# Performance work log

Hardware: AMD Instinct MI355X
Metric: run time of the kernel (lower is better)

## Reference

```python
import jax, jax.numpy as jnp
import numpy as np

jax.config.update("jax_enable_x64", True)  # loss accumulates int64 squared index diffs (~1e14)

PATCH, STRIDE = 7, 1


def extract_patches(img, p, s):
    # img: [b, c, h, w] -> patches [b, N, c*p*p], N = oh*ow (normalize_patch='none')
    pat = jax.lax.conv_general_dilated_patches(img, (p, p), (s, s), 'VALID')  # [b, c*p*p, oh, ow]
    b, d = pat.shape[0], pat.shape[1]
    return pat.reshape(b, d, -1).transpose(0, 2, 1)


def bisect_left(a, v):
    # Exact replica of np.searchsorted(a, v, side='left') binary search,
    # applied (as in the original code) to an UNSORTED int array `a`.
    # a: [N] int, v: [M] int -> [M] insertion indices in [0, N].
    N = a.shape[0]
    lo = jnp.zeros(v.shape, jnp.int64)
    hi = jnp.full(v.shape, N, jnp.int64)
    n_iter = int(np.ceil(np.log2(N))) + 1
    for _ in range(n_iter):
        mid = (lo + hi) // 2
        am = a[jnp.clip(mid, 0, N - 1)]
        go = lo < hi
        pred = am < v
        lo = jnp.where(go & pred, mid + 1, lo)
        hi = jnp.where(go & (~pred), mid, hi)
    return lo


def nearest_vals(a, v):
    # Vectorized find_nearest(a, v_i) for all v_i. a: [N], v: [M].
    N = a.shape[0]
    idx = bisect_left(a, v)
    a_prev = a[jnp.clip(idx - 1, 0, N - 1)]
    a_at = a[jnp.clip(idx, 0, N - 1)]
    take_prev = (idx > 0) & ((idx == N) | (jnp.abs(v - a_prev) < jnp.abs(v - a_at)))
    return jnp.where(take_prev, a_prev, a_at)


def reference(x, y, rand):
    # rand: [b, d, num_proj]; per-batch projection matrix, normalized by unbiased column std
    rand = rand / jnp.std(rand, axis=1, keepdims=True, ddof=1)
    xp = extract_patches(x, PATCH, STRIDE)  # [b, N, d]
    yp = extract_patches(y, PATCH, STRIDE)  # [b, N, d]
    proj_x = jnp.einsum('bnd,bdp->bnp', xp, rand)
    proj_y = jnp.einsum('bnd,bdp->bnp', yp, rand)
    # Original overwrites projections with argsort indices; only j=0 is used
    # because of the early return inside the projection loop.
    ai = jnp.argsort(proj_x[:, :, 0], axis=1).astype(jnp.int64)  # [b, N]
    at = jnp.argsort(proj_y[:, :, 0], axis=1).astype(jnp.int64)  # [b, N]
    nearest = jax.vmap(nearest_vals)(at, ai)  # [b, N]
    N = ai.shape[1]
    per_image = jnp.sum((ai - nearest) ** 2, axis=1) / N  # int sum -> float
    return jnp.mean(per_image)  # batch_reduction='mean'


def setup_inputs() -> dict:
    key = jax.random.key(0)
    k1, k2, k3 = jax.random.split(key, 3)
    b, c, h, w = 4, 3, 256, 256
    d = c * PATCH * PATCH  # 147
    x = jax.random.normal(k1, (b, c, h, w), dtype=jnp.float32)
    y = jax.random.normal(k2, (b, c, h, w), dtype=jnp.float32)
    rand = jax.random.normal(k3, (b, d, 1), dtype=jnp.float32)
    return {"x": x, "y": y, "rand": rand}
```

## Files before the change

kernel.cpp:

```cpp
#include <hip/hip_runtime.h>
#include <stdint.h>

#define OH 250
#define OW 250
#define NPTS (OH*OW)
#define NSEG 4
#define D 147
#define CH 3
#define IMH 256
#define IMW 256
#define NITER 17
#define NBUCK 4096
#define CAP 256
#define SIG0 12.124355652982141

typedef unsigned long long u64;
typedef unsigned int u32;

#define OFF_SREC  0UL
#define OFF_A     33554432UL
#define OFF_CTRL  34554432UL
#define OFF_CURS  34554432UL
#define OFF_SUMS  34619968UL
#define OFF_OFLOW 34620000UL
#define CTRL_LEN  65572UL
#define OFF_BASES 34620008UL
#define WS_NEED   34685560UL

__device__ __forceinline__ u64 packd(double f) {
  u64 u = (u64)__double_as_longlong(f);
  return (u & 0x8000000000000000ULL) ? ~u : (u | 0x8000000000000000ULL);
}

__device__ __forceinline__ int bucket_of(u64 rec) {
  u64 t = rec & ~0x1FFFFULL;
  u64 bits = (t & 0x8000000000000000ULL) ? (t & 0x7FFFFFFFFFFFFFFFULL) : ~t;
  double v = __longlong_as_double((long long)bits);
  double z = (v + 4.0 * SIG0) * ((double)NBUCK / (8.0 * SIG0));
  int b = (z <= 0.0) ? 0 : (int)z;
  if (b > NBUCK - 1) b = NBUCK - 1;
  return b;
}

__global__ __launch_bounds__(256) void conv_kern(const float* __restrict__ y,
                                                 const float* __restrict__ rnd,
                                                 u64* __restrict__ srec,
                                                 u32* __restrict__ curs,
                                                 u32* __restrict__ oflow) {
  __shared__ float tile[CH][22][22];
  __shared__ double w[D];
  int b = blockIdx.z;
  const float* in = y + (size_t)b * CH * IMH * IMW;
  int bi = blockIdx.y * 16, bj = blockIdx.x * 16;
  int tid = threadIdx.y * 16 + threadIdx.x;
  int lane = tid & 63;

  {
    double v0 = (double)rnd[b * D + lane];
    double v1 = (double)rnd[b * D + lane + 64];
    double v2 = (lane + 128 < D) ? (double)rnd[b * D + lane + 128] : 0.0;
    double sm = v0 + v1 + v2;
    #pragma unroll
    for (int o = 32; o > 0; o >>= 1) sm += __shfl_xor(sm, o, 64);
    double mean = sm / (double)D;
    double d0 = v0 - mean, d1 = v1 - mean;
    double d2 = (lane + 128 < D) ? (v2 - mean) : 0.0;
    double ss = d0 * d0 + d1 * d1 + d2 * d2;
    #pragma unroll
    for (int o = 32; o > 0; o >>= 1) ss += __shfl_xor(ss, o, 64);
    double stdv = sqrt(ss / (double)(D - 1));
    w[lane] = v0 / stdv;
    w[lane + 64] = v1 / stdv;
    if (lane + 128 < D) w[lane + 128] = v2 / stdv;
  }
  for (int c = 0; c < CH; ++c)
    for (int t = tid; t < 22 * 22; t += 256) {
      int rr = t / 22, cc = t - rr * 22;
      int r = bi + rr, col = bj + cc;
      float v = 0.f;
      if (r < IMH && col < IMW) v = in[((size_t)c * IMH + r) * IMW + col];
      tile[c][rr][cc] = v;
    }
  __syncthreads();
  int i = bi + threadIdx.y, j = bj + threadIdx.x;
  if (i < OH && j < OW) {
    double acc = 0.0;
    #pragma unroll
    for (int c = 0; c < CH; ++c)
      #pragma unroll
      for (int ph = 0; ph < 7; ++ph)
        #pragma unroll
        for (int pw = 0; pw < 7; ++pw)
          acc = fma((double)tile[c][threadIdx.y + ph][threadIdx.x + pw],
                    w[c * 49 + ph * 7 + pw], acc);
    int n = i * OW + j;
    u64 rec = (packd(acc) & ~0x1FFFFULL) | (u64)(u32)n;
    int bk = b * NBUCK + bucket_of(rec);
    u32 pos = atomicAdd(&curs[bk], 1u);
    if (pos < CAP) srec[(size_t)bk * CAP + pos] = rec;
    else atomicOr(oflow, 1u);
  }
}

__global__ __launch_bounds__(1024) void scan_kern(const u32* __restrict__ curs,
                                                  u32* __restrict__ bases) {
  __shared__ u32 part[1024];
  int seg = blockIdx.x, t = threadIdx.x;
  u32 c[4];
  #pragma unroll
  for (int m = 0; m < 4; ++m) {
    u32 v = curs[seg * NBUCK + 4 * t + m];
    c[m] = v > CAP ? CAP : v;
  }
  u32 s = c[0] + c[1] + c[2] + c[3];
  part[t] = s;
  __syncthreads();
  for (int off = 1; off < 1024; off <<= 1) {
    u32 v = (t >= off) ? part[t - off] : 0u;
    __syncthreads();
    part[t] += v;
    __syncthreads();
  }
  u32 ex = part[t] - s;
  #pragma unroll
  for (int m = 0; m < 4; ++m) {
    bases[seg * (NBUCK + 1) + 4 * t + m] = ex;
    ex += c[m];
  }
  if (t == 1023) bases[seg * (NBUCK + 1) + NBUCK] = ex;
}

__global__ __launch_bounds__(512) void bsort_kern(const u64* __restrict__ srec,
                                                  const u32* __restrict__ bases,
                                                  u32* __restrict__ a) {
  __shared__ u64 buf[8][CAP];
  int wid = threadIdx.x >> 6, lane = threadIdx.x & 63;
  int B = blockIdx.x * 8 + wid;
  int seg = B >> 12, bk = B & (NBUCK - 1);
  u32 b0 = bases[seg * (NBUCK + 1) + bk];
  u32 b1 = bases[seg * (NBUCK + 1) + bk + 1];
  int n = (int)(b1 - b0);
  const u64* src = srec + (size_t)B * CAP;
  u32* dst = a + (size_t)seg * NPTS + b0;
  for (int i = lane; i < n; i += 64) buf[wid][i] = src[i];
  __syncthreads();
  for (int i = lane; i < n; i += 64) {
    u64 x = buf[wid][i];
    int r = 0;
    for (int j = 0; j < n; ++j) r += (buf[wid][j] < x);
    dst[r] = (u32)(x & 0x1FFFFULL);
  }
}

#define HALF (NSEG * NPTS / 2)
__global__ __launch_bounds__(256) void loss_kern(const u32* __restrict__ a_all,
                                                 u64* __restrict__ sums) {
  __shared__ u64 lsums[NSEG];
  int tid = threadIdx.x;
  if (tid < NSEG) lsums[tid] = 0ULL;
  __syncthreads();
  int g = blockIdx.x * 256 + tid;
  if (g < HALF) {
    int g1 = g + HALF;
    int s0 = g / NPTS, s1 = g1 / NPTS;
    int vv0 = g - s0 * NPTS, vv1 = g1 - s1 * NPTS;
    const u32* A0 = a_all + (size_t)s0 * NPTS;
    const u32* A1 = a_all + (size_t)s1 * NPTS;
    int lo0 = 0, hi0 = NPTS, lo1 = 0, hi1 = NPTS;
    #pragma unroll
    for (int it = 0; it < NITER; ++it) {
      int mid0 = (lo0 + hi0) >> 1, mid1 = (lo1 + hi1) >> 1;
      int cm0 = mid0 > NPTS - 1 ? NPTS - 1 : mid0;
      int cm1 = mid1 > NPTS - 1 ? NPTS - 1 : mid1;
      int am0 = (int)A0[cm0];
      int am1 = (int)A1[cm1];
      if (lo0 < hi0) { if (am0 < vv0) lo0 = mid0 + 1; else hi0 = mid0; }
      if (lo1 < hi1) { if (am1 < vv1) lo1 = mid1 + 1; else hi1 = mid1; }
    }
    {
      int pi = lo0 - 1; if (pi < 0) pi = 0; if (pi > NPTS - 1) pi = NPTS - 1;
      int ci = lo0;     if (ci > NPTS - 1) ci = NPTS - 1;
      int ap = (int)A0[pi], aa = (int)A0[ci];
      int d1 = vv0 - ap; if (d1 < 0) d1 = -d1;
      int d2 = vv0 - aa; if (d2 < 0) d2 = -d2;
      bool tp = (lo0 > 0) && ((lo0 == NPTS) || (d1 < d2));
      long long dd = (long long)(vv0 - (tp ? ap : aa));
      atomicAdd(&lsums[s0], (u64)(dd * dd));
    }
    {
      int pi = lo1 - 1; if (pi < 0) pi = 0; if (pi > NPTS - 1) pi = NPTS - 1;
      int ci = lo1;     if (ci > NPTS - 1) ci = NPTS - 1;
      int ap = (int)A1[pi], aa = (int)A1[ci];
      int d1 = vv1 - ap; if (d1 < 0) d1 = -d1;
      int d2 = vv1 - aa; if (d2 < 0) d2 = -d2;
      bool tp = (lo1 > 0) && ((lo1 == NPTS) || (d1 < d2));
      long long dd = (long long)(vv1 - (tp ? ap : aa));
      atomicAdd(&lsums[s1], (u64)(dd * dd));
    }
  }
  __syncthreads();
  if (tid < NSEG && lsums[tid]) atomicAdd(&sums[tid], lsums[tid]);
}

__global__ void final_kern(const u64* __restrict__ sums, const u32* __restrict__ oflow,
                           float* __restrict__ out) {
  if (threadIdx.x == 0 && blockIdx.x == 0) {
    if (oflow[0]) { out[0] = 8.0e12f; return; }
    double l = 0.0;
    for (int b = 0; b < NSEG; ++b) l += (double)(long long)sums[b] / (double)NPTS;
    out[0] = (float)(l / 4.0);
  }
}

__global__ void guard_kern(float* __restrict__ out) {
  if (threadIdx.x == 0 && blockIdx.x == 0) out[0] = 9.0e12f;
}

extern "C" void kernel_launch(void* const* d_in, const int* in_sizes, int n_in,
                              void* d_out, int out_size, void* d_ws, size_t ws_size,
                              hipStream_t stream) {
  (void)in_sizes; (void)n_in; (void)out_size;
  if (ws_size < WS_NEED) { guard_kern<<<1, 64, 0, stream>>>((float*)d_out); return; }
  const float* y   = (const float*)d_in[1];
  const float* rnd = (const float*)d_in[2];

  char* ws = (char*)d_ws;
  u64* srec   = (u64*)(ws + OFF_SREC);
  u32* aidx   = (u32*)(ws + OFF_A);
  u32* curs   = (u32*)(ws + OFF_CURS);
  u64* sums   = (u64*)(ws + OFF_SUMS);
  u32* oflow  = (u32*)(ws + OFF_OFLOW);
  u32* bases  = (u32*)(ws + OFF_BASES);
  float* out  = (float*)d_out;

  hipMemsetAsync(ws + OFF_CTRL, 0, CTRL_LEN, stream);
  conv_kern<<<dim3(16, 16, NSEG), dim3(16, 16), 0, stream>>>(y, rnd, srec, curs, oflow);
  scan_kern<<<NSEG, 1024, 0, stream>>>(curs, bases);
  bsort_kern<<<NSEG * NBUCK / 8, 512, 0, stream>>>(srec, bases, aidx);
  loss_kern<<<(HALF + 255) / 256, 256, 0, stream>>>(aidx, sums);
  final_kern<<<1, 64, 0, stream>>>(sums, oflow, out);
}
```

Before: 119.3 us.

## Double bucket count, move weight prep to setup kernel, fuse final reduction into loss

Replaces the memset with a setup kernel that zeroes the control buffers and precomputes normalized projection weights once, instead of having every conv block redo the std reduction. Buckets go from 4096 to 8192 with capacity 128, so each per-bucket quadratic rank sort handles fewer elements. The final kernel is folded into the loss kernel through a last-block ticket counter, and a completeness check on the scan total is added. Per-channel partial accumulation changes the FMA order slightly, and the smaller capacity raises the risk of bucket overflow.

```diff
diff --git a/kernel.cpp b/kernel.cpp
--- a/kernel.cpp
+++ b/kernel.cpp
@@ -10,8 +10,8 @@
 #define IMH 256
 #define IMW 256
 #define NITER 17
-#define NBUCK 4096
-#define CAP 256
+#define NBUCK 8192
+#define CAP 128
 #define SIG0 12.124355652982141
 
 typedef unsigned long long u64;
@@ -19,13 +19,13 @@
 
 #define OFF_SREC  0UL
 #define OFF_A     33554432UL
-#define OFF_CTRL  34554432UL
-#define OFF_CURS  34554432UL
-#define OFF_SUMS  34619968UL
-#define OFF_OFLOW 34620000UL
-#define CTRL_LEN  65572UL
-#define OFF_BASES 34620008UL
-#define WS_NEED   34685560UL
+#define OFF_WTS   34554432UL
+#define OFF_CURS  34559136UL
+#define OFF_BASES 34690208UL
+#define OFF_SUMS  34821296UL
+#define OFF_TICK  34821328UL
+#define OFF_OFLOW 34821336UL
+#define WS_NEED   34821340UL
 
 __device__ __forceinline__ u64 packd(double f) {
   u64 u = (u64)__double_as_longlong(f);
@@ -42,20 +42,16 @@
   return b;
 }
 
-__global__ __launch_bounds__(256) void conv_kern(const float* __restrict__ y,
-                                                 const float* __restrict__ rnd,
-                                                 u64* __restrict__ srec,
-                                                 u32* __restrict__ curs,
-                                                 u32* __restrict__ oflow) {
-  __shared__ float tile[CH][22][22];
-  __shared__ double w[D];
-  int b = blockIdx.z;
-  const float* in = y + (size_t)b * CH * IMH * IMW;
-  int bi = blockIdx.y * 16, bj = blockIdx.x * 16;
-  int tid = threadIdx.y * 16 + threadIdx.x;
-  int lane = tid & 63;
-
-  {
+__global__ __launch_bounds__(256) void setup_kern(const float* __restrict__ rnd,
+                                                  double* __restrict__ wts,
+                                                  u32* __restrict__ curs,
+                                                  u64* __restrict__ sums,
+                                                  u32* __restrict__ tick,
+                                                  u32* __restrict__ oflow) {
+  int t = threadIdx.x;
+  if (blockIdx.x < 4) {
+    int b = blockIdx.x;
+    int lane = t & 63;
     double v0 = (double)rnd[b * D + lane];
     double v1 = (double)rnd[b * D + lane + 64];
     double v2 = (lane + 128 < D) ? (double)rnd[b * D + lane + 128] : 0.0;
@@ -69,10 +65,33 @@
     #pragma unroll
     for (int o = 32; o > 0; o >>= 1) ss += __shfl_xor(ss, o, 64);
     double stdv = sqrt(ss / (double)(D - 1));
-    w[lane] = v0 / stdv;
-    w[lane + 64] = v1 / stdv;
-    if (lane + 128 < D) w[lane + 128] = v2 / stdv;
-  }
+    if (t < 64) {
+      wts[b * D + lane] = v0 / stdv;
+      wts[b * D + lane + 64] = v1 / stdv;
+      if (lane + 128 < D) wts[b * D + lane + 128] = v2 / stdv;
+    }
+    if (b == 0 && t < 8) ((u32*)sums)[t] = 0u;
+    if (b == 0 && t >= 8 && t < 10) tick[t - 8] = 0u;
+    if (b == 0 && t == 10) oflow[0] = 0u;
+  } else {
+    int g = (blockIdx.x - 4) * 1024 + t * 4;
+    if (g < NSEG * NBUCK) {
+      curs[g] = 0u; curs[g + 1] = 0u; curs[g + 2] = 0u; curs[g + 3] = 0u;
+    }
+  }
+}
+
+__global__ __launch_bounds__(256) void conv_kern(const float* __restrict__ y,
+                                                 const double* __restrict__ wts,
+                                                 u64* __restrict__ srec,
+                                                 u32* __restrict__ curs,
+                                                 u32* __restrict__ oflow) {
+  __shared__ float tile[CH][22][22];
+  int b = blockIdx.z;
+  const float* in = y + (size_t)b * CH * IMH * IMW;
+  const double* wb = wts + b * D;
+  int bi = blockIdx.y * 16, bj = blockIdx.x * 16;
+  int tid = threadIdx.y * 16 + threadIdx.x;
   for (int c = 0; c < CH; ++c)
     for (int t = tid; t < 22 * 22; t += 256) {
       int rr = t / 22, cc = t - rr * 22;
@@ -86,13 +105,16 @@
   if (i < OH && j < OW) {
     double acc = 0.0;
     #pragma unroll
-    for (int c = 0; c < CH; ++c)
+    for (int c = 0; c < CH; ++c) {
+      double ac = 0.0;
       #pragma unroll
       for (int ph = 0; ph < 7; ++ph)
         #pragma unroll
         for (int pw = 0; pw < 7; ++pw)
-          acc = fma((double)tile[c][threadIdx.y + ph][threadIdx.x + pw],
-                    w[c * 49 + ph * 7 + pw], acc);
+          ac = fma((double)tile[c][threadIdx.y + ph][threadIdx.x + pw],
+                   wb[c * 49 + ph * 7 + pw], ac);
+      acc += ac;
+    }
     int n = i * OW + j;
     u64 rec = (packd(acc) & ~0x1FFFFULL) | (u64)(u32)n;
     int bk = b * NBUCK + bucket_of(rec);
@@ -103,17 +125,18 @@
 }
 
 __global__ __launch_bounds__(1024) void scan_kern(const u32* __restrict__ curs,
-                                                  u32* __restrict__ bases) {
+                                                  u32* __restrict__ bases,
+                                                  u32* __restrict__ oflow) {
   __shared__ u32 part[1024];
   int seg = blockIdx.x, t = threadIdx.x;
-  u32 c[4];
+  u32 c[8]; u32 run = 0;
   #pragma unroll
-  for (int m = 0; m < 4; ++m) {
-    u32 v = curs[seg * NBUCK + 4 * t + m];
+  for (int m = 0; m < 8; ++m) {
+    u32 v = curs[seg * NBUCK + 8 * t + m];
     c[m] = v > CAP ? CAP : v;
-  }
-  u32 s = c[0] + c[1] + c[2] + c[3];
-  part[t] = s;
+    run += c[m];
+  }
+  part[t] = run;
   __syncthreads();
   for (int off = 1; off < 1024; off <<= 1) {
     u32 v = (t >= off) ? part[t - off] : 0u;
@@ -121,13 +144,16 @@
     part[t] += v;
     __syncthreads();
   }
-  u32 ex = part[t] - s;
+  u32 ex = part[t] - run;
   #pragma unroll
-  for (int m = 0; m < 4; ++m) {
-    bases[seg * (NBUCK + 1) + 4 * t + m] = ex;
+  for (int m = 0; m < 8; ++m) {
+    bases[seg * (NBUCK + 1) + 8 * t + m] = ex;
     ex += c[m];
   }
-  if (t == 1023) bases[seg * (NBUCK + 1) + NBUCK] = ex;
+  if (t == 1023) {
+    bases[seg * (NBUCK + 1) + NBUCK] = ex;
+    if (ex != NPTS) atomicOr(oflow, 2u);
+  }
 }
 
 __global__ __launch_bounds__(512) void bsort_kern(const u64* __restrict__ srec,
@@ -136,7 +162,7 @@
   __shared__ u64 buf[8][CAP];
   int wid = threadIdx.x >> 6, lane = threadIdx.x & 63;
   int B = blockIdx.x * 8 + wid;
-  int seg = B >> 12, bk = B & (NBUCK - 1);
+  int seg = B / NBUCK, bk = B & (NBUCK - 1);
   u32 b0 = bases[seg * (NBUCK + 1) + bk];
   u32 b1 = bases[seg * (NBUCK + 1) + bk + 1];
   int n = (int)(b1 - b0);
@@ -154,8 +180,13 @@
 
 #define HALF (NSEG * NPTS / 2)
 __global__ __launch_bounds__(256) void loss_kern(const u32* __restrict__ a_all,
-                                                 u64* __restrict__ sums) {
+                                                 u64* __restrict__ sums,
+                                                 u32* __restrict__ tick,
+                                                 const u32* __restrict__ oflow,
+                                                 float* __restrict__ out,
+                                                 int nblocks) {
   __shared__ u64 lsums[NSEG];
+  __shared__ u32 rank_s;
   int tid = threadIdx.x;
   if (tid < NSEG) lsums[tid] = 0ULL;
   __syncthreads();
@@ -200,15 +231,19 @@
   }
   __syncthreads();
   if (tid < NSEG && lsums[tid]) atomicAdd(&sums[tid], lsums[tid]);
-}
-
-__global__ void final_kern(const u64* __restrict__ sums, const u32* __restrict__ oflow,
-                           float* __restrict__ out) {
-  if (threadIdx.x == 0 && blockIdx.x == 0) {
-    if (oflow[0]) { out[0] = 8.0e12f; return; }
-    double l = 0.0;
-    for (int b = 0; b < NSEG; ++b) l += (double)(long long)sums[b] / (double)NPTS;
-    out[0] = (float)(l / 4.0);
+  __syncthreads();
+  if (tid == 0) {
+    rank_s = atomicAdd(&tick[1], 1u);
+    if (rank_s == (u32)(nblocks - 1)) {
+      u32 of = __hip_atomic_load(oflow, __ATOMIC_RELAXED, __HIP_MEMORY_SCOPE_AGENT);
+      if (of) { out[0] = 8.0e12f + 1.0e11f * (float)of; return; }
+      double l = 0.0;
+      for (int s = 0; s < NSEG; ++s) {
+        u64 sv = __hip_atomic_load(&sums[s], __ATOMIC_RELAXED, __HIP_MEMORY_SCOPE_AGENT);
+        l += (double)(long long)sv / (double)NPTS;
+      }
+      out[0] = (float)(l / 4.0);
+    }
   }
 }
 
@@ -227,16 +262,18 @@
   char* ws = (char*)d_ws;
   u64* srec   = (u64*)(ws + OFF_SREC);
   u32* aidx   = (u32*)(ws + OFF_A);
+  double* wts = (double*)(ws + OFF_WTS);
   u32* curs   = (u32*)(ws + OFF_CURS);
+  u32* bases  = (u32*)(ws + OFF_BASES);
   u64* sums   = (u64*)(ws + OFF_SUMS);
+  u32* tick   = (u32*)(ws + OFF_TICK);
   u32* oflow  = (u32*)(ws + OFF_OFLOW);
-  u32* bases  = (u32*)(ws + OFF_BASES);
   float* out  = (float*)d_out;
 
-  hipMemsetAsync(ws + OFF_CTRL, 0, CTRL_LEN, stream);
-  conv_kern<<<dim3(16, 16, NSEG), dim3(16, 16), 0, stream>>>(y, rnd, srec, curs, oflow);
-  scan_kern<<<NSEG, 1024, 0, stream>>>(curs, bases);
+  setup_kern<<<36, 256, 0, stream>>>(rnd, wts, curs, sums, tick, oflow);
+  conv_kern<<<dim3(16, 16, NSEG), dim3(16, 16), 0, stream>>>(y, wts, srec, curs, oflow);
+  scan_kern<<<NSEG, 1024, 0, stream>>>(curs, bases, oflow);
   bsort_kern<<<NSEG * NBUCK / 8, 512, 0, stream>>>(srec, bases, aidx);
-  loss_kern<<<(HALF + 255) / 256, 256, 0, stream>>>(aidx, sums);
-  final_kern<<<1, 64, 0, stream>>>(sums, oflow, out);
-}
+  int nb = (HALF + 255) / 256;
+  loss_kern<<<nb, 256, 0, stream>>>(aidx, sums, tick, oflow, out, nb);
+}
```

Result: no change. 118.2 us, median of 2 (-0.9%).
